# Kernel optimization log

Measured on AMD Instinct MI355X. Metric: run time of the kernel, lower is better.

## Reference

```python
import jax, jax.numpy as jnp
import numpy as np

B, S, V = 64, 128, 5000
D_TEXT, D_AUDIO, D_VIDEO = 300, 74, 35
H_LSTM = 128
C = 16            # contracted dim per modality
M = C ** 3        # measurement_dim = 4096
UNITS = 256       # measurement_size
CELL = 64         # output_cell_dim


def setup_inputs():
    key = jax.random.key(0)
    ks = jax.random.split(key, 24)
    def n(k, shape, s=0.05):
        return jax.random.normal(k, shape, jnp.float32) * s
    return {
        "text_idx": jax.random.randint(ks[0], (B, S), 0, V),
        "audio": jax.random.normal(ks[1], (B, S, D_AUDIO), jnp.float32),
        "video": jax.random.normal(ks[2], (B, S, D_VIDEO), jnp.float32),
        "embed_table": n(ks[3], (V, D_TEXT), 0.1),
        "phase_tables": jax.random.uniform(ks[4], (3, V, C), jnp.float32, -np.pi, np.pi),
        "lstm_Wih": n(ks[5], (4 * H_LSTM, D_TEXT)),
        "lstm_Whh": n(ks[6], (4 * H_LSTM, H_LSTM)),
        "lstm_bih": jnp.zeros((4 * H_LSTM,), jnp.float32),
        "lstm_bhh": jnp.zeros((4 * H_LSTM,), jnp.float32),
        "text_proj_W": n(ks[7], (C, H_LSTM)), "text_proj_b": jnp.zeros((C,), jnp.float32),
        "aud_W1": n(ks[8], (C, D_AUDIO)), "aud_b1": jnp.zeros((C,), jnp.float32),
        "aud_W2": n(ks[9], (C, C)), "aud_b2": jnp.zeros((C,), jnp.float32),
        "aud_W3": n(ks[10], (C, C)), "aud_b3": jnp.zeros((C,), jnp.float32),
        "vid_W1": n(ks[11], (C, D_VIDEO)), "vid_b1": jnp.zeros((C,), jnp.float32),
        "vid_W2": n(ks[12], (C, C)), "vid_b2": jnp.zeros((C,), jnp.float32),
        "vid_W3": n(ks[13], (C, C)), "vid_b3": jnp.zeros((C,), jnp.float32),
        "modality_weights": jnp.zeros((3,), jnp.float32),
        "meas_kr": n(ks[14], (UNITS, M), 1.0),
        "meas_ki": n(ks[15], (UNITS, M), 1.0),
        "fc1_W": n(ks[16], (CELL, UNITS)), "fc1_b": jnp.zeros((CELL,), jnp.float32),
        "fc2_W": n(ks[17], (CELL, CELL)), "fc2_b": jnp.zeros((CELL,), jnp.float32),
        "fc3_W": n(ks[18], (1, CELL)), "fc3_b": jnp.zeros((1,), jnp.float32),
    }


def _lstm(x, Wih, Whh, bih, bhh):
    # torch nn.LSTMCell over time (gate order i, f, g, o)
    b = x.shape[0]
    h_dim = Whh.shape[1]
    def step(carry, xt):
        h, c = carry
        g = xt @ Wih.T + bih + h @ Whh.T + bhh
        i, f, gg, o = jnp.split(g, 4, axis=-1)
        c = jax.nn.sigmoid(f) * c + jax.nn.sigmoid(i) * jnp.tanh(gg)
        h = jax.nn.sigmoid(o) * jnp.tanh(c)
        return (h, c), h
    init = (jnp.zeros((b, h_dim), x.dtype), jnp.zeros((b, h_dim), x.dtype))
    _, hs = jax.lax.scan(step, init, jnp.swapaxes(x, 0, 1))
    return jnp.swapaxes(hs, 0, 1)  # (B,S,H)


def _mlp(x, W1, b1, W2, b2, W3, b3):
    y = jax.nn.relu(x @ W1.T + b1)
    y = jax.nn.relu(y @ W2.T + b2)
    return jax.nn.relu(y @ W3.T + b3)


def _kron_complex(tr, ti, hr, hi):
    # (tr + i*ti) (x) (hr + i*hi), matching torch bmm(tp.unsqueeze(2), h.unsqueeze(1)).view(B,-1)
    rr = jnp.einsum('bsa,bsd->bsad', tr, hr) - jnp.einsum('bsa,bsd->bsad', ti, hi)
    ri = jnp.einsum('bsa,bsd->bsad', tr, hi) + jnp.einsum('bsa,bsd->bsad', ti, hr)
    b, s = tr.shape[:2]
    return rr.reshape(b, s, -1), ri.reshape(b, s, -1)


def _forward(text_idx, audio, video, embed_table, phase_tables,
             lstm_Wih, lstm_Whh, lstm_bih, lstm_bhh, text_proj_W, text_proj_b,
             aud_W1, aud_b1, aud_W2, aud_b2, aud_W3, aud_b3,
             vid_W1, vid_b1, vid_W2, vid_b2, vid_W3, vid_b3,
             modality_weights, meas_kr, meas_ki,
             fc1_W, fc1_b, fc2_W, fc2_b, fc3_W, fc3_b):
    text = embed_table[text_idx]                                   # (B,S,300)
    amp_text = _lstm(text, lstm_Wih, lstm_Whh, lstm_bih, lstm_bhh) @ text_proj_W.T + text_proj_b
    amp_aud = _mlp(audio, aud_W1, aud_b1, aud_W2, aud_b2, aud_W3, aud_b3)
    amp_vid = _mlp(video, vid_W1, vid_b1, vid_W2, vid_b2, vid_W3, vid_b3)

    hr, hi, wts = [], [], []
    for i, a in enumerate([amp_text, amp_aud, amp_vid]):
        norm = jnp.linalg.norm(a, axis=-1, keepdims=True)          # (B,S,1)
        a_n = a / norm                                             # L2Normalization
        wts.append(jax.nn.softmax(norm, axis=1))                   # softmax over sequence
        ph = phase_tables[i][text_idx]                             # (B,S,C)
        hr.append(jnp.cos(ph) * a_n)                               # ComplexMultiply
        hi.append(jnp.sin(ph) * a_n)

    mw = jax.nn.softmax(modality_weights)
    weight = mw[0] * wts[0] + mw[1] * wts[1] + mw[2] * wts[2]      # (B,S,1)

    # tensor (Kronecker) product across modalities; NOTE: imag initialized to ONES as in source
    tr = jnp.ones((text_idx.shape[0], text_idx.shape[1], 1), amp_text.dtype)
    ti = jnp.ones_like(tr)
    for r, im in zip(hr, hi):
        tr, ti = _kron_complex(tr, ti, r, im)                      # -> (B,S,M)

    # complex self-attention (Q=K=V=per-token product states)
    Ur = jnp.einsum('bsd,btd->bst', tr, tr) - jnp.einsum('bsd,btd->bst', ti, ti)
    Ui = jnp.einsum('bsd,btd->bst', ti, tr) + jnp.einsum('bsd,btd->bst', tr, ti)
    ar = jax.nn.softmax(Ur, axis=2)
    ai = jax.nn.softmax(Ui, axis=2)
    out_r = jnp.einsum('bst,btd->bsd', ar, tr) - jnp.einsum('bst,btd->bsd', ai, ti) + tr
    out_i = jnp.einsum('bst,btd->bsd', ai, tr) + jnp.einsum('bst,btd->bsd', ar, ti) + ti

    # ComplexMeasurement2: normalized complex projectors, weighted sum of |<k|psi>|^2 over seq
    kn = jnp.sqrt(jnp.sum(meas_kr ** 2 + meas_ki ** 2, axis=-1, keepdims=True))
    kr = meas_kr / kn
    ki = meas_ki / kn
    inr = out_r @ kr.T + out_i @ ki.T                              # (B,S,UNITS)
    ini = out_i @ kr.T - out_r @ ki.T
    prob = inr ** 2 + ini ** 2
    meas = jnp.sum(weight * prob, axis=1)                          # (B,UNITS)

    y = jax.nn.relu(meas @ fc1_W.T + fc1_b)
    y = jax.nn.relu(y @ fc2_W.T + fc2_b)
    return y @ fc3_W.T + fc3_b                                     # (B,1)


def reference(text_idx, audio, video, embed_table, phase_tables,
              lstm_Wih, lstm_Whh, lstm_bih, lstm_bhh, text_proj_W, text_proj_b,
              aud_W1, aud_b1, aud_W2, aud_b2, aud_W3, aud_b3,
              vid_W1, vid_b1, vid_W2, vid_b2, vid_W3, vid_b3,
              modality_weights, meas_kr, meas_ki,
              fc1_W, fc1_b, fc2_W, fc2_b, fc3_W, fc3_b):
    return _forward(text_idx, audio, video, embed_table, phase_tables,
                    lstm_Wih, lstm_Whh, lstm_bih, lstm_bhh, text_proj_W, text_proj_b,
                    aud_W1, aud_b1, aud_W2, aud_b2, aud_W3, aud_b3,
                    vid_W1, vid_b1, vid_W2, vid_b2, vid_W3, vid_b3,
                    modality_weights, meas_kr, meas_ki,
                    fc1_W, fc1_b, fc2_W, fc2_b, fc3_W, fc3_b)
```

## Files before the change

### kernel.cpp

```cpp
#include <hip/hip_runtime.h>
#include <math.h>

constexpr int B = 64, S = 128, V = 5000;
constexpr int DT = 300, DA = 74, DV = 35;
constexpr int H = 128, C16 = 16;
constexpr int Mdim = 4096, UNITS = 256;
constexpr int T_ = B * S;
constexpr int NCH = 128;

typedef __attribute__((ext_vector_type(8))) short short8v;
typedef __attribute__((ext_vector_type(4))) float f32x4;
typedef _Float16 half2v __attribute__((ext_vector_type(2)));

__device__ __forceinline__ unsigned short f2bf(float x) {
    unsigned int u = __float_as_uint(x);
    unsigned int r = (u + 0x7fffu + ((u >> 16) & 1u)) >> 16;
    return (unsigned short)r;
}
__device__ __forceinline__ float bf2f(unsigned short h) {
    return __uint_as_float(((unsigned int)h) << 16);
}
__device__ __forceinline__ float fsig(float x) { return 1.f / (1.f + __expf(-x)); }
__device__ __forceinline__ float ftanh(float x) {
    float t = __expf(2.f * x);
    return (t - 1.f) / (t + 1.f);
}

union U2 { unsigned int u; half2v v; };

__global__ __launch_bounds__(256, 2) void k_embed(const int* __restrict__ idx,
                                                  const float* __restrict__ emb,
                                                  const float* __restrict__ Wih,
                                                  const float* __restrict__ bih,
                                                  const float* __restrict__ bhh,
                                                  float* __restrict__ xW) {
    __shared__ float As[60][132];
    __shared__ float Ws[60][132];
    __shared__ int sidx[128];
    int tid = threadIdx.x;
    int t0 = (blockIdx.x >> 2) * 128;
    int j0 = (blockIdx.x & 3) * 128;
    if (tid < 128) sidx[tid] = idx[t0 + tid];

    int jq = tid & 15, tq = tid >> 4;
    float acc[8][8];
#pragma unroll
    for (int r = 0; r < 8; r++)
#pragma unroll
        for (int cc = 0; cc < 8; cc++) acc[r][cc] = 0.f;

    __syncthreads();
    for (int c = 0; c < 5; c++) {
        int k0 = c * 60;
        if (c) __syncthreads();
        for (int i = tid; i < 128 * 60; i += 256) {
            int tok = i / 60, kk = i - tok * 60;
            As[kk][tok] = emb[(size_t)sidx[tok] * 300 + k0 + kk];
            Ws[kk][tok] = Wih[(size_t)(j0 + tok) * 300 + k0 + kk];
        }
        __syncthreads();
#pragma unroll 4
        for (int kk = 0; kk < 60; kk++) {
            float4 a0 = *(const float4*)&As[kk][tq * 8];
            float4 a1 = *(const float4*)&As[kk][tq * 8 + 4];
            float4 w0 = *(const float4*)&Ws[kk][jq * 8];
            float4 w1 = *(const float4*)&Ws[kk][jq * 8 + 4];
            float a[8] = {a0.x, a0.y, a0.z, a0.w, a1.x, a1.y, a1.z, a1.w};
            float w[8] = {w0.x, w0.y, w0.z, w0.w, w1.x, w1.y, w1.z, w1.w};
#pragma unroll
            for (int r = 0; r < 8; r++)
#pragma unroll
                for (int cc = 0; cc < 8; cc++)
                    acc[r][cc] = fmaf(a[r], w[cc], acc[r][cc]);
        }
    }
    float bb[8];
#pragma unroll
    for (int cc = 0; cc < 8; cc++) {
        int j = j0 + jq * 8 + cc;
        bb[cc] = bih[j] + bhh[j];
    }
#pragma unroll
    for (int r = 0; r < 8; r++) {
        int t = t0 + tq * 8 + r;
        float4 o0, o1;
        o0.x = acc[r][0] + bb[0]; o0.y = acc[r][1] + bb[1];
        o0.z = acc[r][2] + bb[2]; o0.w = acc[r][3] + bb[3];
        o1.x = acc[r][4] + bb[4]; o1.y = acc[r][5] + bb[5];
        o1.z = acc[r][6] + bb[6]; o1.w = acc[r][7] + bb[7];
        *(float4*)&xW[(size_t)t * 512 + j0 + jq * 8] = o0;
        *(float4*)&xW[(size_t)t * 512 + j0 + jq * 8 + 4] = o1;
    }
}

__global__ __launch_bounds__(256) void k_lstm(const float* __restrict__ xW,
                                              const float* __restrict__ Whh,
                                              float* __restrict__ hs) {
    __shared__ __align__(16) unsigned int hsm[2][64];
    int b = blockIdx.x, tid = threadIdx.x;
    int ch = tid >> 1, gp = tid & 1;
    int g0 = gp * 2, g1 = gp * 2 + 1;

    unsigned int wA[64], wB[64];
    const float* wr0 = Whh + (size_t)(g0 * 128 + ch) * 128;
    const float* wr1 = Whh + (size_t)(g1 * 128 + ch) * 128;
#pragma unroll
    for (int k = 0; k < 64; k++) {
        U2 t;
        t.v[0] = (_Float16)wr0[2 * k];
        t.v[1] = (_Float16)wr0[2 * k + 1];
        wA[k] = t.u;
        U2 u;
        u.v[0] = (_Float16)wr1[2 * k];
        u.v[1] = (_Float16)wr1[2 * k + 1];
        wB[k] = u.u;
    }
    if (tid < 64) { hsm[0][tid] = 0u; hsm[1][tid] = 0u; }

    const float* xwb = xW + (size_t)b * S * 512;
    float* hb = hs + (size_t)b * S * H;
    int gch0 = g0 * 128 + ch, gch1 = g1 * 128 + ch;
    float xn0 = xwb[gch0], xn1 = xwb[gch1];
    float c = 0.f;
    __syncthreads();

    int cur = 0;
    for (int s = 0; s < S; s++) {
        float xc0 = xn0, xc1 = xn1;
        if (s + 1 < S) {
            xn0 = xwb[(size_t)(s + 1) * 512 + gch0];
            xn1 = xwb[(size_t)(s + 1) * 512 + gch1];
        }
        float a0 = 0.f, a1 = 0.f, a2 = 0.f, a3 = 0.f;
        float b0 = 0.f, b1 = 0.f, b2 = 0.f, b3 = 0.f;
#pragma unroll
        for (int kb = 0; kb < 16; kb++) {
            uint4 hv = *(const uint4*)&hsm[cur][kb * 4];
            U2 h0, h1, h2, h3;
            h0.u = hv.x; h1.u = hv.y; h2.u = hv.z; h3.u = hv.w;
            U2 xa0, xa1, xa2, xa3, xb0, xb1, xb2, xb3;
            xa0.u = wA[kb * 4];     xa1.u = wA[kb * 4 + 1];
            xa2.u = wA[kb * 4 + 2]; xa3.u = wA[kb * 4 + 3];
            xb0.u = wB[kb * 4];     xb1.u = wB[kb * 4 + 1];
            xb2.u = wB[kb * 4 + 2]; xb3.u = wB[kb * 4 + 3];
#if __has_builtin(__builtin_amdgcn_fdot2)
            a0 = __builtin_amdgcn_fdot2(h0.v, xa0.v, a0, false);
            a1 = __builtin_amdgcn_fdot2(h1.v, xa1.v, a1, false);
            a2 = __builtin_amdgcn_fdot2(h2.v, xa2.v, a2, false);
            a3 = __builtin_amdgcn_fdot2(h3.v, xa3.v, a3, false);
            b0 = __builtin_amdgcn_fdot2(h0.v, xb0.v, b0, false);
            b1 = __builtin_amdgcn_fdot2(h1.v, xb1.v, b1, false);
            b2 = __builtin_amdgcn_fdot2(h2.v, xb2.v, b2, false);
            b3 = __builtin_amdgcn_fdot2(h3.v, xb3.v, b3, false);
#else
            a0 = fmaf((float)h0.v[0], (float)xa0.v[0], fmaf((float)h0.v[1], (float)xa0.v[1], a0));
            a1 = fmaf((float)h1.v[0], (float)xa1.v[0], fmaf((float)h1.v[1], (float)xa1.v[1], a1));
            a2 = fmaf((float)h2.v[0], (float)xa2.v[0], fmaf((float)h2.v[1], (float)xa2.v[1], a2));
            a3 = fmaf((float)h3.v[0], (float)xa3.v[0], fmaf((float)h3.v[1], (float)xa3.v[1], a3));
            b0 = fmaf((float)h0.v[0], (float)xb0.v[0], fmaf((float)h0.v[1], (float)xb0.v[1], b0));
            b1 = fmaf((float)h1.v[0], (float)xb1.v[0], fmaf((float)h1.v[1], (float)xb1.v[1], b1));
            b2 = fmaf((float)h2.v[0], (float)xb2.v[0], fmaf((float)h2.v[1], (float)xb2.v[1], b2));
            b3 = fmaf((float)h3.v[0], (float)xb3.v[0], fmaf((float)h3.v[1], (float)xb3.v[1], b3));
#endif
        }
        float pre0 = xc0 + ((a0 + a1) + (a2 + a3));
        float pre1 = xc1 + ((b0 + b1) + (b2 + b3));
        float sA = __shfl_xor(pre0, 1);
        float sB = __shfl_xor(pre1, 1);
        float gi = gp ? sA : pre0;
        float gf = gp ? sB : pre1;
        float gg = gp ? pre0 : sA;
        float go = gp ? pre1 : sB;
        c = fsig(gf) * c + fsig(gi) * ftanh(gg);
        float hval = fsig(go) * ftanh(c);
        int nxt = cur ^ 1;
        if (gp == 0) {
            ((_Float16*)&hsm[nxt][0])[ch] = (_Float16)hval;
            hb[s * H + ch] = hval;
        }
        __syncthreads();
        cur = nxt;
    }
}

__global__ __launch_bounds__(256) void k_amp_kprep(const float* __restrict__ hs,
                                                   const float* __restrict__ audio,
                                                   const float* __restrict__ video,
                                                   const float* __restrict__ pW, const float* __restrict__ pb,
                                                   const float* __restrict__ aW1, const float* __restrict__ ab1,
                                                   const float* __restrict__ aW2, const float* __restrict__ ab2,
                                                   const float* __restrict__ aW3, const float* __restrict__ ab3,
                                                   const float* __restrict__ vW1, const float* __restrict__ vb1,
                                                   const float* __restrict__ vW2, const float* __restrict__ vb2,
                                                   const float* __restrict__ vW3, const float* __restrict__ vb3,
                                                   float* __restrict__ ampT, float* __restrict__ ampA,
                                                   float* __restrict__ ampV,
                                                   const float* __restrict__ kr,
                                                   const float* __restrict__ ki,
                                                   unsigned short* __restrict__ Bh) {
    __shared__ float sPW[16 * 128], sA1[16 * 74], sV1[16 * 35];
    __shared__ float sA2[256], sA3[256], sV2[256], sV3[256];
    __shared__ float sbp[16], sba1[16], sba2[16], sba3[16], sbv1[16], sbv2[16], sbv3[16];
    __shared__ float red[256];
    int tid = threadIdx.x;

    if (blockIdx.x >= 32) {
        int u = blockIdx.x - 32;
        const float* r0 = kr + (size_t)u * Mdim;
        const float* i0 = ki + (size_t)u * Mdim;
        float ss = 0.f;
        for (int d = tid; d < Mdim; d += 256) {
            float a = r0[d], b2 = i0[d];
            ss = fmaf(a, a, fmaf(b2, b2, ss));
        }
        red[tid] = ss; __syncthreads();
        for (int off = 128; off > 0; off >>= 1) {
            if (tid < off) red[tid] += red[tid + off];
            __syncthreads();
        }
        float inv = 1.f / sqrtf(red[0]);
        for (int d = tid; d < Mdim; d += 256) {
            float xr = r0[d] * inv, xi = i0[d] * inv;
            unsigned short hr = f2bf(xr);
            unsigned short hi_ = f2bf(xi);
            int ch = d >> 5;
            int kl = (d & 31) * 2;
            size_t base = ((size_t)ch * 512 + 2 * u) * 64 + kl;
            Bh[base] = hr;  Bh[base + 1] = hi_;
            size_t base2 = base + 64;
            Bh[base2] = hi_ ^ 0x8000; Bh[base2 + 1] = hr;
        }
        return;
    }

    for (int i = tid; i < 16 * 128; i += 256) sPW[i] = pW[i];
    for (int i = tid; i < 16 * 74; i += 256) sA1[i] = aW1[i];
    for (int i = tid; i < 16 * 35; i += 256) sV1[i] = vW1[i];
    if (tid < 256) { sA2[tid] = aW2[tid]; sA3[tid] = aW3[tid]; sV2[tid] = vW2[tid]; sV3[tid] = vW3[tid]; }
    if (tid < 16) {
        sbp[tid] = pb[tid];
        sba1[tid] = ab1[tid]; sba2[tid] = ab2[tid]; sba3[tid] = ab3[tid];
        sbv1[tid] = vb1[tid]; sbv2[tid] = vb2[tid]; sbv3[tid] = vb3[tid];
    }
    __syncthreads();
    int t = blockIdx.x * 256 + tid;

    const float* hrow = hs + (size_t)t * H;
    float accT[16];
#pragma unroll
    for (int m = 0; m < 16; m++) accT[m] = sbp[m];
    for (int k = 0; k < 128; k += 4) {
        float4 hv = *(const float4*)&hrow[k];
#pragma unroll
        for (int m = 0; m < 16; m++) {
            float4 wv = *(const float4*)&sPW[m * 128 + k];
            accT[m] = fmaf(hv.x, wv.x, fmaf(hv.y, wv.y, fmaf(hv.z, wv.z, fmaf(hv.w, wv.w, accT[m]))));
        }
    }
#pragma unroll
    for (int m = 0; m < 16; m++) ampT[t * 16 + m] = accT[m];

    float y1[16], y2[16];
    const float* arow = audio + (size_t)t * DA;
#pragma unroll 4
    for (int m = 0; m < 16; m++) {
        float a = sba1[m];
        for (int k = 0; k < DA; k++) a = fmaf(arow[k], sA1[m * DA + k], a);
        y1[m] = fmaxf(a, 0.f);
    }
#pragma unroll
    for (int m = 0; m < 16; m++) {
        float a = sba2[m];
#pragma unroll
        for (int k = 0; k < 16; k++) a = fmaf(y1[k], sA2[m * 16 + k], a);
        y2[m] = fmaxf(a, 0.f);
    }
#pragma unroll
    for (int m = 0; m < 16; m++) {
        float a = sba3[m];
#pragma unroll
        for (int k = 0; k < 16; k++) a = fmaf(y2[k], sA3[m * 16 + k], a);
        ampA[t * 16 + m] = fmaxf(a, 0.f);
    }
    const float* vrow = video + (size_t)t * DV;
#pragma unroll 4
    for (int m = 0; m < 16; m++) {
        float a = sbv1[m];
        for (int k = 0; k < DV; k++) a = fmaf(vrow[k], sV1[m * DV + k], a);
        y1[m] = fmaxf(a, 0.f);
    }
#pragma unroll
    for (int m = 0; m < 16; m++) {
        float a = sbv2[m];
#pragma unroll
        for (int k = 0; k < 16; k++) a = fmaf(y1[k], sV2[m * 16 + k], a);
        y2[m] = fmaxf(a, 0.f);
    }
#pragma unroll
    for (int m = 0; m < 16; m++) {
        float a = sbv3[m];
#pragma unroll
        for (int k = 0; k < 16; k++) a = fmaf(y2[k], sV3[m * 16 + k], a);
        ampV[t * 16 + m] = fmaxf(a, 0.f);
    }
}

__global__ __launch_bounds__(128) void k_modality(const int* __restrict__ idx,
                                                  const float* __restrict__ pt,
                                                  const float* __restrict__ ampT,
                                                  const float* __restrict__ ampA,
                                                  const float* __restrict__ ampV,
                                                  const float* __restrict__ mweights,
                                                  float* __restrict__ zq, float* __restrict__ wt) {
    int b = blockIdx.x, s = threadIdx.x;
    __shared__ float red[128];
    int t = b * S + s;
    const float* amps0 = ampT + (size_t)t * 16;
    const float* amps1 = ampA + (size_t)t * 16;
    const float* amps2 = ampV + (size_t)t * 16;

    float m0 = mweights[0], m1 = mweights[1], m2 = mweights[2];
    float mx = fmaxf(m0, fmaxf(m1, m2));
    float e0 = expf(m0 - mx), e1 = expf(m1 - mx), e2 = expf(m2 - mx);
    float es = e0 + e1 + e2;
    float mw[3] = {e0 / es, e1 / es, e2 / es};

    int row = idx[t];
    float wacc = 0.f;
    for (int m = 0; m < 3; m++) {
        const float* amp = (m == 0) ? amps0 : (m == 1) ? amps1 : amps2;
        float av[16];
        float ss = 0.f;
#pragma unroll
        for (int c2 = 0; c2 < 16; c2++) { av[c2] = amp[c2]; ss = fmaf(av[c2], av[c2], ss); }
        float nrm = sqrtf(ss);
        red[s] = nrm; __syncthreads();
        for (int off = 64; off > 0; off >>= 1) {
            if (s < off) red[s] = fmaxf(red[s], red[s + off]);
            __syncthreads();
        }
        float rmax = red[0]; __syncthreads();
        float ex = expf(nrm - rmax);
        red[s] = ex; __syncthreads();
        for (int off = 64; off > 0; off >>= 1) {
            if (s < off) red[s] += red[s + off];
            __syncthreads();
        }
        float rsum = red[0]; __syncthreads();
        wacc = fmaf(mw[m], ex / rsum, wacc);

        float inv = 1.f / nrm;
        const float* ph = pt + ((size_t)m * V + row) * 16;
        float2* zdst = (float2*)zq + ((size_t)m * T_ + t) * 16;
#pragma unroll
        for (int c2 = 0; c2 < 16; c2++) {
            float an = av[c2] * inv;
            float p = ph[c2];
            zdst[c2] = make_float2(cosf(p) * an, sinf(p) * an);
        }
    }
    wt[t] = wacc;
}

__global__ __launch_bounds__(256, 2) void k_gmalpha(const float* __restrict__ zq,
                                                    const unsigned short* __restrict__ Bh,
                                                    unsigned int* __restrict__ Gt32,
                                                    unsigned int* __restrict__ ahq,
                                                    unsigned int* __restrict__ alq) {
    __shared__ __align__(16) unsigned char smem[55296];
    int tid = threadIdx.x;

    if (blockIdx.x < 512) {
        int xcd = blockIdx.x & 7;
        int nt = xcd >> 1;
        int mt = ((blockIdx.x >> 3) << 1) | (xcd & 1);
        int t0 = mt * 64, n0 = nt * 128;

        int tl = tid >> 2, qf = tid & 3;
        int tok = t0 + tl;
        int h = qf >> 1;
        int d3b = (qf & 1) * 8;
        const float2* zq2 = (const float2*)zq;
        float z3r[8], z3i[8];
#pragma unroll
        for (int j = 0; j < 8; j++) {
            float2 v = zq2[((size_t)2 * T_ + tok) * 16 + d3b + j];
            z3r[j] = v.x; z3i[j] = v.y;
        }

        int wid = tid >> 6, lane = tid & 63;
        int wn = wid >> 1, wt2 = wid & 1;
        int lrow = lane & 15, lk = lane >> 4;

        f32x4 acc[4][2];
#pragma unroll
        for (int fm = 0; fm < 4; fm++)
#pragma unroll
            for (int fn = 0; fn < 2; fn++) acc[fm][fn] = (f32x4){0.f, 0.f, 0.f, 0.f};

        union S8 { short8v v; unsigned short u[8]; };

        for (int cp = 0; cp < NCH / 2; cp++) {
            uint4 bvh[2][4];
#pragma unroll
            for (int sc = 0; sc < 2; sc++) {
                int ch = 2 * cp + sc;
                const unsigned short* srcH = Bh + ((size_t)ch * 512 + n0) * 64;
#pragma unroll
                for (int l = 0; l < 4; l++) {
                    int i2 = tid + 256 * l;
                    bvh[sc][l] = *(const uint4*)(srcH + (size_t)i2 * 8);
                }
            }

#pragma unroll
            for (int sc = 0; sc < 2; sc++) {
                int ch = 2 * cp + sc;
                unsigned short (*Ah)[72] = (unsigned short (*)[72])(smem + sc * 9216);
                unsigned short (*Bhs)[72] = (unsigned short (*)[72])(smem + 18432 + sc * 18432);
                int d1 = ch >> 3;
                int d2 = ((ch & 7) << 1) + h;
                float2 z1 = zq2[(size_t)tok * 16 + d1];
                float2 z2 = zq2[((size_t)T_ + tok) * 16 + d2];
                float w1r = z1.x - z1.y, w1i = z1.x + z1.y;
                float wr_ = w1r * z2.x - w1i * z2.y;
                float wi_ = w1r * z2.y + w1i * z2.x;
                S8 h0, h1;
#pragma unroll
                for (int j = 0; j < 8; j++) {
                    float pr_ = wr_ * z3r[j] - wi_ * z3i[j];
                    float pi_ = wr_ * z3i[j] + wi_ * z3r[j];
                    unsigned short phr = f2bf(pr_);
                    unsigned short phi = f2bf(pi_);
                    if (j < 4) {
                        h0.u[2 * j] = phr;     h0.u[2 * j + 1] = phi;
                    } else {
                        h1.u[2 * (j - 4)] = phr; h1.u[2 * (j - 4) + 1] = phi;
                    }
                }
                int aoff = h * 32 + (qf & 1) * 16;
                *(short8v*)&Ah[tl][aoff] = h0.v;
                *(short8v*)&Ah[tl][aoff + 8] = h1.v;
#pragma unroll
                for (int l = 0; l < 4; l++) {
                    int i2 = tid + 256 * l;
                    *(uint4*)&Bhs[i2 >> 3][(i2 & 7) * 8] = bvh[sc][l];
                }
            }
            __syncthreads();

#pragma unroll
            for (int sc = 0; sc < 2; sc++) {
                unsigned short (*Ah)[72] = (unsigned short (*)[72])(smem + sc * 9216);
                unsigned short (*Bhs)[72] = (unsigned short (*)[72])(smem + 18432 + sc * 18432);
#pragma unroll
                for (int kk = 0; kk < 2; kk++) {
                    short8v kf[4], ahf[2];
#pragma unroll
                    for (int fm = 0; fm < 4; fm++) {
                        int nr = wn * 64 + fm * 16 + lrow;
                        int co = kk * 32 + lk * 8;
                        kf[fm] = *(const short8v*)&Bhs[nr][co];
                    }
#pragma unroll
                    for (int fn = 0; fn < 2; fn++) {
                        int ro = wt2 * 32 + fn * 16 + lrow;
                        int co = kk * 32 + lk * 8;
                        ahf[fn] = *(const short8v*)&Ah[ro][co];
                    }
#pragma unroll
                    for (int fm = 0; fm < 4; fm++)
#pragma unroll
                        for (int fn = 0; fn < 2; fn++)
                            acc[fm][fn] = __builtin_amdgcn_mfma_f32_16x16x32_bf16(kf[fm], ahf[fn], acc[fm][fn], 0, 0, 0);
                }
            }
            __syncthreads();
        }

#pragma unroll
        for (int fm = 0; fm < 4; fm++)
#pragma unroll
            for (int fn = 0; fn < 2; fn++) {
                int t = t0 + wt2 * 32 + fn * 16 + lrow;
                int bb = t >> 7, tl2 = t & 127;
#pragma unroll
                for (int p = 0; p < 2; p++) {
                    int ng = n0 + wn * 64 + fm * 16 + lk * 4 + 2 * p;
                    float vr = acc[fm][fn][2 * p];
                    float vi = acc[fm][fn][2 * p + 1];
                    unsigned int evenw = (unsigned int)f2bf(vr) | ((unsigned int)f2bf(-vi) << 16);
                    unsigned int oddw  = (unsigned int)f2bf(vi) | ((unsigned int)f2bf(vr) << 16);
                    Gt32[((size_t)bb * 512 + ng) * 128 + tl2] = evenw;
                    Gt32[((size_t)bb * 512 + ng + 1) * 128 + tl2] = oddw;
                }
            }
        return;
    }

    float* zs = (float*)smem;
    int bidx = blockIdx.x - 512;
    int b = bidx >> 3, s0 = (bidx & 7) * 16;
    int sl = tid >> 4, tg = tid & 15;

    for (int i = tid; i < 3 * 128 * 32; i += 256) {
        int m = i >> 12;
        int rem = i & 4095;
        int tok = rem >> 5, jj = rem & 31;
        zs[(m * 128 + tok) * 34 + jj] = zq[((size_t)m * T_ + b * S) * 32 + rem];
    }
    __syncthreads();

    int s = s0 + sl;
    float pr[8], pi[8];
#pragma unroll
    for (int j = 0; j < 8; j++) { pr[j] = 1.f; pi[j] = 0.f; }
    for (int m = 0; m < 3; m++) {
        float sr_[16], si_[16];
        const float* zss = &zs[(m * 128 + s) * 34];
#pragma unroll
        for (int c2 = 0; c2 < 16; c2++) { sr_[c2] = zss[2 * c2]; si_[c2] = zss[2 * c2 + 1]; }
#pragma unroll
        for (int j = 0; j < 8; j++) {
            int t = tg + 16 * j;
            const float* zst = &zs[(m * 128 + t) * 34];
            float dr = 0.f, di = 0.f;
#pragma unroll
            for (int c2 = 0; c2 < 16; c2++) {
                float br_ = zst[2 * c2], bi_ = zst[2 * c2 + 1];
                dr = fmaf(sr_[c2], br_, fmaf(-si_[c2], bi_, dr));
                di = fmaf(sr_[c2], bi_, fmaf(si_[c2], br_, di));
            }
            float nr = pr[j] * dr - pi[j] * di;
            float ni = pr[j] * di + pi[j] * dr;
            pr[j] = nr; pi[j] = ni;
        }
    }
    float ur[8], ui[8];
#pragma unroll
    for (int j = 0; j < 8; j++) { ur[j] = -2.f * pi[j]; ui[j] = 2.f * pr[j]; }

    float mr = ur[0], mi_ = ui[0];
#pragma unroll
    for (int j = 1; j < 8; j++) { mr = fmaxf(mr, ur[j]); mi_ = fmaxf(mi_, ui[j]); }
    for (int off = 1; off < 16; off <<= 1) {
        mr = fmaxf(mr, __shfl_xor(mr, off));
        mi_ = fmaxf(mi_, __shfl_xor(mi_, off));
    }
    float sr = 0.f, si = 0.f;
#pragma unroll
    for (int j = 0; j < 8; j++) {
        ur[j] = expf(ur[j] - mr); sr += ur[j];
        ui[j] = expf(ui[j] - mi_); si += ui[j];
    }
    for (int off = 1; off < 16; off <<= 1) {
        sr += __shfl_xor(sr, off);
        si += __shfl_xor(si, off);
    }
    float invr = 1.f / sr, invi = 1.f / si;
    unsigned int* ah_ = ahq + ((size_t)b * S + s) * 128;
    unsigned int* al_ = alq + ((size_t)b * S + s) * 128;
#pragma unroll
    for (int j = 0; j < 8; j++) {
        int t = tg + 16 * j;
        float arj = ur[j] * invr;
        float aij = ui[j] * invi;
        if (t == s) arj += 1.f;
        unsigned short rh = f2bf(arj), ih = f2bf(aij);
        unsigned short rl = f2bf(arj - bf2f(rh)), il = f2bf(aij - bf2f(ih));
        ah_[t] = (unsigned int)rh | ((unsigned int)ih << 16);
        al_[t] = (unsigned int)rl | ((unsigned int)il << 16);
    }
}

__global__ __launch_bounds__(256, 2) void k_meas_mfma(const unsigned short* __restrict__ Aq,
                                                      const unsigned short* __restrict__ Alq,
                                                      const unsigned short* __restrict__ Gt,
                                                      const float* __restrict__ wt,
                                                      float* __restrict__ meas) {
    int tid = threadIdx.x;
    int b = blockIdx.x >> 2, nq = blockIdx.x & 3;
    int wid = tid >> 6, lane = tid & 63;
    int ws = wid >> 1, wn2 = wid & 1;
    int lrow = lane & 15, lk = lane >> 4;

    f32x4 acc[4][4];
#pragma unroll
    for (int fm = 0; fm < 4; fm++)
#pragma unroll
        for (int fn = 0; fn < 4; fn++) acc[fm][fn] = (f32x4){0.f, 0.f, 0.f, 0.f};

    const unsigned short* Ab = Aq + (size_t)b * 128 * 256;
    const unsigned short* Alb = Alq + (size_t)b * 128 * 256;
    const unsigned short* Gb = Gt + (size_t)b * 512 * 256;

    for (int kc = 0; kc < 8; kc++) {
        int ko = kc * 32 + lk * 8;
        short8v ah[4], al[4], bt[4];
#pragma unroll
        for (int fm = 0; fm < 4; fm++) {
            int s = ws * 64 + fm * 16 + lrow;
            ah[fm] = *(const short8v*)(Ab + (size_t)s * 256 + ko);
            al[fm] = *(const short8v*)(Alb + (size_t)s * 256 + ko);
        }
#pragma unroll
        for (int fn = 0; fn < 4; fn++) {
            int n = nq * 128 + wn2 * 64 + fn * 16 + lrow;
            bt[fn] = *(const short8v*)(Gb + (size_t)n * 256 + ko);
        }
#pragma unroll
        for (int fm = 0; fm < 4; fm++)
#pragma unroll
            for (int fn = 0; fn < 4; fn++) {
                acc[fm][fn] = __builtin_amdgcn_mfma_f32_16x16x32_bf16(ah[fm], bt[fn], acc[fm][fn], 0, 0, 0);
                acc[fm][fn] = __builtin_amdgcn_mfma_f32_16x16x32_bf16(al[fm], bt[fn], acc[fm][fn], 0, 0, 0);
            }
    }

    __shared__ float red[4][4][16];
    float part[4] = {0.f, 0.f, 0.f, 0.f};
#pragma unroll
    for (int fm = 0; fm < 4; fm++)
#pragma unroll
        for (int j = 0; j < 4; j++) {
            int s = ws * 64 + fm * 16 + lk * 4 + j;
            float w = wt[b * S + s];
#pragma unroll
            for (int fn = 0; fn < 4; fn++) {
                float v = acc[fm][fn][j];
                part[fn] = fmaf(w * v, v, part[fn]);
            }
        }
#pragma unroll
    for (int fn = 0; fn < 4; fn++) {
        part[fn] += __shfl_xor(part[fn], 16);
        part[fn] += __shfl_xor(part[fn], 32);
    }
    if (lane < 16) {
#pragma unroll
        for (int fn = 0; fn < 4; fn++) red[wid][fn][lane] = part[fn];
    }
    __syncthreads();
    if (tid < 64) {
        int n0 = 2 * tid;
        int wn2a = n0 >> 6, rem = n0 & 63, fna = rem >> 4, ca = rem & 15;
        float v = red[wn2a][fna][ca] + red[2 + wn2a][fna][ca]
                + red[wn2a][fna][ca + 1] + red[2 + wn2a][fna][ca + 1];
        meas[(size_t)b * UNITS + nq * 64 + tid] = v;
    }
}

__global__ __launch_bounds__(64) void k_head(const float* __restrict__ meas,
                                             const float* __restrict__ fc1W, const float* __restrict__ fc1b,
                                             const float* __restrict__ fc2W, const float* __restrict__ fc2b,
                                             const float* __restrict__ fc3W, const float* __restrict__ fc3b,
                                             float* __restrict__ out) {
    int b = blockIdx.x, j = threadIdx.x;
    __shared__ float y[64];
    float a = fc1b[j];
    for (int u = 0; u < 256; u++) a = fmaf(meas[(size_t)b * 256 + u], fc1W[j * 256 + u], a);
    y[j] = fmaxf(a, 0.f);
    __syncthreads();
    float a2 = fc2b[j];
#pragma unroll
    for (int k = 0; k < 64; k++) a2 = fmaf(y[k], fc2W[j * 64 + k], a2);
    a2 = fmaxf(a2, 0.f);
    float v = a2 * fc3W[j];
    for (int off = 32; off > 0; off >>= 1) v += __shfl_down(v, off);
    if (j == 0) out[b] = v + fc3b[0];
}

extern "C" void kernel_launch(void* const* d_in, const int* in_sizes, int n_in,
                              void* d_out, int out_size, void* d_ws, size_t ws_size,
                              hipStream_t stream) {
    const int* text_idx = (const int*)d_in[0];
    const float* audio = (const float*)d_in[1];
    const float* video = (const float*)d_in[2];
    const float* emb = (const float*)d_in[3];
    const float* pt = (const float*)d_in[4];
    const float* Wih = (const float*)d_in[5];
    const float* Whh = (const float*)d_in[6];
    const float* bih = (const float*)d_in[7];
    const float* bhh = (const float*)d_in[8];
    const float* pW = (const float*)d_in[9];
    const float* pb = (const float*)d_in[10];
    const float* aW1 = (const float*)d_in[11];
    const float* ab1 = (const float*)d_in[12];
    const float* aW2 = (const float*)d_in[13];
    const float* ab2 = (const float*)d_in[14];
    const float* aW3 = (const float*)d_in[15];
    const float* ab3 = (const float*)d_in[16];
    const float* vW1 = (const float*)d_in[17];
    const float* vb1 = (const float*)d_in[18];
    const float* vW2 = (const float*)d_in[19];
    const float* vb2 = (const float*)d_in[20];
    const float* vW3 = (const float*)d_in[21];
    const float* vb3 = (const float*)d_in[22];
    const float* mweights = (const float*)d_in[23];
    const float* mkr = (const float*)d_in[24];
    const float* mki = (const float*)d_in[25];
    const float* fc1W = (const float*)d_in[26];
    const float* fc1b = (const float*)d_in[27];
    const float* fc2W = (const float*)d_in[28];
    const float* fc2b = (const float*)d_in[29];
    const float* fc3W = (const float*)d_in[30];
    const float* fc3b = (const float*)d_in[31];

    float* ws = (float*)d_ws;
    size_t off = 0;
    float* hs = ws + off;   off += (size_t)T_ * H;
    float* xW = ws + off;   off += (size_t)T_ * 512;
    float* ampT = ws + off; off += (size_t)T_ * 16;
    float* ampA = ws + off; off += (size_t)T_ * 16;
    float* ampV = ws + off; off += (size_t)T_ * 16;
    float* zq = ws + off;   off += (size_t)3 * T_ * 32;
    float* wt = ws + off;   off += (size_t)T_;
    unsigned short* BhW = (unsigned short*)(ws + off); off += (size_t)2097152;
    unsigned int* ahq = (unsigned int*)(ws + off); off += (size_t)1048576;
    unsigned int* alq = (unsigned int*)(ws + off); off += (size_t)1048576;
    float* meas = ws + off; off += (size_t)B * UNITS;
    (void)ws_size; (void)in_sizes; (void)n_in; (void)out_size;

    k_embed<<<256, 256, 0, stream>>>(text_idx, emb, Wih, bih, bhh, xW);
    k_lstm<<<B, 256, 0, stream>>>(xW, Whh, hs);
    k_amp_kprep<<<288, 256, 0, stream>>>(hs, audio, video, pW, pb,
                                         aW1, ab1, aW2, ab2, aW3, ab3,
                                         vW1, vb1, vW2, vb2, vW3, vb3,
                                         ampT, ampA, ampV,
                                         mkr, mki, BhW);
    k_modality<<<B, 128, 0, stream>>>(text_idx, pt, ampT, ampA, ampV, mweights, zq, wt);
    k_gmalpha<<<1024, 256, 0, stream>>>(zq, BhW, (unsigned int*)xW , ahq, alq);
    k_meas_mfma<<<256, 256, 0, stream>>>((const unsigned short*)ahq,
                                         (const unsigned short*)alq,
                                         (const unsigned short*)xW ,
                                         wt, meas);
    k_head<<<B, 64, 0, stream>>>(meas, fc1W, fc1b, fc2W, fc2b, fc3W, fc3b, (float*)d_out);
}
```

Before: 377.3 us.

## Build A-operand MFMA fragments directly in registers instead of via LDS

The kernel now computes the tensor-product A operand (z1*z2*z3 outer products) in the exact lane layout the bf16 MFMA expects, holding it in registers instead of writing it to shared memory and reading it back. This removes the A-tile LDS stores and loads and shrinks shared memory use. In exchange, each wave computes its own A fragments, so the outer-product arithmetic and bf16 conversion are duplicated across the two waves that share a token tile, and register pressure rises.

New measurement: 497.9 us. +31.9%, slower.

```diff
diff --git a/kernel.cpp b/kernel.cpp
--- a/kernel.cpp
+++ b/kernel.cpp
@@ -367,7 +367,7 @@
                                                     unsigned int* __restrict__ Gt32,
                                                     unsigned int* __restrict__ ahq,
                                                     unsigned int* __restrict__ alq) {
-    __shared__ __align__(16) unsigned char smem[55296];
+    __shared__ __align__(16) unsigned char smem[52224];
     int tid = threadIdx.x;
 
     if (blockIdx.x < 512) {
@@ -376,21 +376,21 @@
         int mt = ((blockIdx.x >> 3) << 1) | (xcd & 1);
         int t0 = mt * 64, n0 = nt * 128;
 
-        int tl = tid >> 2, qf = tid & 3;
-        int tok = t0 + tl;
-        int h = qf >> 1;
-        int d3b = (qf & 1) * 8;
-        const float2* zq2 = (const float2*)zq;
-        float z3r[8], z3i[8];
-#pragma unroll
-        for (int j = 0; j < 8; j++) {
-            float2 v = zq2[((size_t)2 * T_ + tok) * 16 + d3b + j];
-            z3r[j] = v.x; z3i[j] = v.y;
-        }
-
         int wid = tid >> 6, lane = tid & 63;
         int wn = wid >> 1, wt2 = wid & 1;
         int lrow = lane & 15, lk = lane >> 4;
+        const float2* zq2 = (const float2*)zq;
+
+        int tokA0 = t0 + wt2 * 32 + lrow;
+        int tokA1 = tokA0 + 16;
+        float z3r[2][4], z3i[2][4];
+#pragma unroll
+        for (int j = 0; j < 4; j++) {
+            float2 v0 = zq2[((size_t)2 * T_ + tokA0) * 16 + lk * 4 + j];
+            float2 v1 = zq2[((size_t)2 * T_ + tokA1) * 16 + lk * 4 + j];
+            z3r[0][j] = v0.x; z3i[0][j] = v0.y;
+            z3r[1][j] = v1.x; z3i[1][j] = v1.y;
+        }
 
         f32x4 acc[4][2];
 #pragma unroll
@@ -413,34 +413,36 @@
                 }
             }
 
+            S8 areg[2][2][2];
 #pragma unroll
             for (int sc = 0; sc < 2; sc++) {
                 int ch = 2 * cp + sc;
-                unsigned short (*Ah)[72] = (unsigned short (*)[72])(smem + sc * 9216);
-                unsigned short (*Bhs)[72] = (unsigned short (*)[72])(smem + 18432 + sc * 18432);
                 int d1 = ch >> 3;
-                int d2 = ((ch & 7) << 1) + h;
-                float2 z1 = zq2[(size_t)tok * 16 + d1];
-                float2 z2 = zq2[((size_t)T_ + tok) * 16 + d2];
-                float w1r = z1.x - z1.y, w1i = z1.x + z1.y;
-                float wr_ = w1r * z2.x - w1i * z2.y;
-                float wi_ = w1r * z2.y + w1i * z2.x;
-                S8 h0, h1;
-#pragma unroll
-                for (int j = 0; j < 8; j++) {
-                    float pr_ = wr_ * z3r[j] - wi_ * z3i[j];
-                    float pi_ = wr_ * z3i[j] + wi_ * z3r[j];
-                    unsigned short phr = f2bf(pr_);
-                    unsigned short phi = f2bf(pi_);
-                    if (j < 4) {
-                        h0.u[2 * j] = phr;     h0.u[2 * j + 1] = phi;
-                    } else {
-                        h1.u[2 * (j - 4)] = phr; h1.u[2 * (j - 4) + 1] = phi;
+#pragma unroll
+                for (int fn = 0; fn < 2; fn++) {
+                    int tok = fn ? tokA1 : tokA0;
+                    float2 z1 = zq2[(size_t)tok * 16 + d1];
+                    float w1r = z1.x - z1.y, w1i = z1.x + z1.y;
+#pragma unroll
+                    for (int kk = 0; kk < 2; kk++) {
+                        int d2 = ((ch & 7) << 1) + kk;
+                        float2 z2 = zq2[((size_t)T_ + tok) * 16 + d2];
+                        float wr_ = w1r * z2.x - w1i * z2.y;
+                        float wi_ = w1r * z2.y + w1i * z2.x;
+#pragma unroll
+                        for (int j = 0; j < 4; j++) {
+                            float pr_ = wr_ * z3r[fn][j] - wi_ * z3i[fn][j];
+                            float pi_ = wr_ * z3i[fn][j] + wi_ * z3r[fn][j];
+                            areg[sc][fn][kk].u[2 * j] = f2bf(pr_);
+                            areg[sc][fn][kk].u[2 * j + 1] = f2bf(pi_);
+                        }
                     }
                 }
-                int aoff = h * 32 + (qf & 1) * 16;
-                *(short8v*)&Ah[tl][aoff] = h0.v;
-                *(short8v*)&Ah[tl][aoff + 8] = h1.v;
+            }
+
+#pragma unroll
+            for (int sc = 0; sc < 2; sc++) {
+                unsigned short (*Bhs)[72] = (unsigned short (*)[72])(smem + sc * 18432);
 #pragma unroll
                 for (int l = 0; l < 4; l++) {
                     int i2 = tid + 256 * l;
@@ -451,11 +453,10 @@
 
 #pragma unroll
             for (int sc = 0; sc < 2; sc++) {
-                unsigned short (*Ah)[72] = (unsigned short (*)[72])(smem + sc * 9216);
-                unsigned short (*Bhs)[72] = (unsigned short (*)[72])(smem + 18432 + sc * 18432);
+                unsigned short (*Bhs)[72] = (unsigned short (*)[72])(smem + sc * 18432);
 #pragma unroll
                 for (int kk = 0; kk < 2; kk++) {
-                    short8v kf[4], ahf[2];
+                    short8v kf[4];
 #pragma unroll
                     for (int fm = 0; fm < 4; fm++) {
                         int nr = wn * 64 + fm * 16 + lrow;
@@ -463,16 +464,10 @@
                         kf[fm] = *(const short8v*)&Bhs[nr][co];
                     }
 #pragma unroll
-                    for (int fn = 0; fn < 2; fn++) {
-                        int ro = wt2 * 32 + fn * 16 + lrow;
-                        int co = kk * 32 + lk * 8;
-                        ahf[fn] = *(const short8v*)&Ah[ro][co];
-                    }
-#pragma unroll
                     for (int fm = 0; fm < 4; fm++)
 #pragma unroll
                         for (int fn = 0; fn < 2; fn++)
-                            acc[fm][fn] = __builtin_amdgcn_mfma_f32_16x16x32_bf16(kf[fm], ahf[fn], acc[fm][fn], 0, 0, 0);
+                            acc[fm][fn] = __builtin_amdgcn_mfma_f32_16x16x32_bf16(kf[fm], areg[sc][fn][kk].v, acc[fm][fn], 0, 0, 0);
                 }
             }
             __syncthreads();
```
